# Kernel tuning notes

Measured on AMD Instinct MI355X. Metric: run time of the kernel, lower is better.

The kernel has to match this reference:

```python
import jax, jax.numpy as jnp
import numpy as np

ITERS = 8
LAMBDA0 = 0.01
PAD = 1.0
LR = 1.0
EPS = 1e-12


def _sobel_grads(fmap):
    # kornia spatial_gradient: normalized 3x3 sobel (/8), replicate padding. fmap: C,H,W
    kx = jnp.array([[-1., 0., 1.], [-2., 0., 2.], [-1., 0., 1.]], fmap.dtype) / 8.0
    k = jnp.stack([kx, kx.T])[:, None]                       # 2,1,3,3 (OIHW)
    f = jnp.pad(fmap, ((0, 0), (1, 1), (1, 1)), mode='edge')[:, None]  # C,1,H+2,W+2
    g = jax.lax.conv_general_dilated(f, k, (1, 1), 'VALID')  # C,2,H,W
    return g[:, 0], g[:, 1]


def _bilinear(tensor, pts):
    # grid_sample bilinear, align_corners=True, at pixel coords. tensor: C,H,W; pts: N,2 (x,y) -> N,C
    c, h, w = tensor.shape
    x, y = pts[:, 0], pts[:, 1]
    x0 = jnp.clip(jnp.floor(x), 0, w - 1)
    y0 = jnp.clip(jnp.floor(y), 0, h - 1)
    x1 = jnp.clip(x0 + 1, 0, w - 1)
    y1 = jnp.clip(y0 + 1, 0, h - 1)
    wx, wy = x - x0, y - y0
    x0i, x1i = x0.astype(jnp.int32), x1.astype(jnp.int32)
    y0i, y1i = y0.astype(jnp.int32), y1.astype(jnp.int32)
    v00 = tensor[:, y0i, x0i]
    v01 = tensor[:, y0i, x1i]
    v10 = tensor[:, y1i, x0i]
    v11 = tensor[:, y1i, x1i]
    out = (v00 * (1 - wx) * (1 - wy) + v01 * wx * (1 - wy)
           + v10 * (1 - wx) * wy + v11 * wx * wy)
    return out.T


def _skew(v):
    x, y, z = v[..., 0], v[..., 1], v[..., 2]
    o = jnp.zeros_like(x)
    return jnp.stack([o, -z, y, z, o, -x, -y, x, o], -1).reshape(v.shape[:-1] + (3, 3))


def _so3exp(w):
    theta = jnp.linalg.norm(w)
    small = theta < 1e-7
    th = jnp.where(small, 1.0, theta)
    A = jnp.where(small, 1.0, jnp.sin(th) / th)
    B = jnp.where(small, 0.5, (1.0 - jnp.cos(th)) / th ** 2)
    W = _skew(w)
    return jnp.eye(3, dtype=w.dtype) + A * W + B * (W @ W)


def _normalize(x):
    return x / jnp.maximum(jnp.linalg.norm(x, axis=-1, keepdims=True), EPS)


def _pnp(p3D, feature_ref, feature_query, K, R_init, t_init):
    C, H, W = feature_query.shape
    gx, gy = _sobel_grads(feature_query)
    fref = _normalize(feature_ref)
    fx, fy, cx, cy = K[0, 0], K[1, 1], K[0, 2], K[1, 2]
    f_scale = jnp.stack([fx, fy])
    c_off = jnp.stack([cx, cy])

    def project(R, t):
        p3q = p3D @ R.T + t
        pn = p3q[:, :2] / p3q[:, 2:3]
        return p3q, pn, pn * f_scale + c_off

    def in_image(p2):
        return ((p2[:, 0] >= PAD) & (p2[:, 0] < W - PAD)
                & (p2[:, 1] >= PAD) & (p2[:, 1] < H - PAD))

    def masked_cost(p2, vf):
        f = _normalize(_bilinear(feature_query, p2))
        cost = ((f - fref) ** 2).sum(-1)
        return (cost * vf).sum() / vf.sum()

    R, t = R_init, t_init
    lam = jnp.asarray(LAMBDA0, p3D.dtype)
    jacobi = None
    cost_best = None
    p2D_init = None

    for i in range(ITERS):
        p3q, pn, p2 = project(R, t)
        if i == 0:
            p2D_init = jax.lax.stop_gradient(p2)
        vf = in_image(p2).astype(p3D.dtype)  # mask-weight == gather of valid pts

        f_raw = _bilinear(feature_query, p2)  # N,C
        norm = jnp.maximum(jnp.linalg.norm(f_raw, axis=-1, keepdims=True), EPS)
        f = f_raw / norm
        error = f - fref
        if i == 0:
            cost_best = (((error ** 2).sum(-1)) * vf).sum() / vf.sum()

        # Jacobian chain: J = J_f_p2 @ J_p2_pn @ J_pn_p3 @ J_p3_T   -> N,C,6
        x_, y_, d = p3q[:, 0], p3q[:, 1], p3q[:, 2]
        z = jnp.zeros_like(d)
        Jpn = jnp.stack([1 / d, z, -x_ / d ** 2,
                         z, 1 / d, -y_ / d ** 2], -1).reshape(-1, 2, 3)
        Jpn = Jpn * f_scale[None, :, None]  # fold in J_p2_pn = diag(fx,fy)
        Jp3T = jnp.concatenate(
            [jnp.broadcast_to(jnp.eye(3, dtype=p3D.dtype), p3q.shape[:-1] + (3, 3)),
             -_skew(p3q)], -1)  # N,3,6
        J26 = Jpn @ Jp3T       # N,2,6

        Jf = jnp.stack([_bilinear(gx, p2), _bilinear(gy, p2)], -1)  # N,C,2
        # normalize-feat Jacobian (I - f f^T)/||f_raw||, fused (no NxCxC)
        proj = jnp.einsum('nc,nck->nk', f, Jf)
        Jf = (Jf - f[:, :, None] * proj[:, None, :]) / norm[:, :, None]

        J = Jf @ J26  # N,C,6
        if i == 0:
            jacobi = 1.0 / (1.0 + jnp.linalg.norm(J * vf[:, None, None], axis=(0, 1)))
        J = J * jacobi

        Grad = jnp.einsum('ncj,nc,n->j', J, error, vf)
        Hess = jnp.einsum('nci,ncj,n->ij', J, J, vf)

        damp = jnp.diag(jnp.diagonal(Hess) + 1e-9) * lam  # LM damping
        delta = -LR * jnp.linalg.solve(Hess + damp, Grad)
        delta = delta * jacobi
        dt, dw = delta[:3], delta[3:6]
        dr = _so3exp(dw)
        R_new, t_new = dr @ R, dr @ t + dt

        _, _, p2_new = project(R_new, t_new)
        vf_new = in_image(p2_new).astype(p3D.dtype)
        cost_new = masked_cost(p2_new, vf_new)

        accept = cost_new <= cost_best
        lam = jnp.clip(lam * jnp.where(accept, 0.1, 10.0), 1e-8, 1e4)
        R = jnp.where(accept, R_new, R)
        t = jnp.where(accept, t_new, t)
        cost_best = jnp.where(accept, cost_new, cost_best)

    p3D_sg = jax.lax.stop_gradient(p3D)
    pf = p3D_sg @ R.T + t
    p2f = (pf[:, :2] / pf[:, 2:3]) * f_scale + c_off
    f_i = _normalize(_bilinear(feature_query, p2D_init))
    f_f = _normalize(_bilinear(feature_query, p2f))
    cost_init = ((fref - f_i) ** 2).sum(-1)
    cost_final = ((fref - f_f) ** 2).sum(-1)
    nan = jnp.asarray(jnp.nan, cost_init.dtype)
    cost_init = jnp.where(in_image(p2D_init), cost_init, nan)
    cost_final = jnp.where(in_image(p2f), cost_final, nan)
    return R, t, cost_init, cost_final


def setup_inputs() -> dict:
    N, C, H, W = 10000, 128, 512, 512
    key = jax.random.key(0)
    ks = jax.random.split(key, 4)
    xy = jax.random.uniform(ks[0], (N, 2), jnp.float32, -2.0, 2.0)
    z = jax.random.uniform(ks[1], (N, 1), jnp.float32, 4.0, 10.0)
    p3D = jnp.concatenate([xy, z], -1)
    feature_query = jax.random.normal(ks[2], (C, H, W), jnp.float32) * 0.5
    feature_ref = jax.random.normal(ks[3], (N, C), jnp.float32)
    K = jnp.array([[500., 0., 256.], [0., 500., 256.], [0., 0., 1.]], jnp.float32)
    R_init = _so3exp(jnp.array([0.01, -0.02, 0.015], jnp.float32))
    t_init = jnp.array([0.05, -0.03, 0.10], jnp.float32)
    return {"p3D": p3D, "feature_ref": feature_ref, "feature_query": feature_query,
            "K": K, "R_init": R_init, "t_init": t_init}


def reference(p3D, feature_ref, feature_query, K, R_init, t_init):
    return _pnp(p3D, feature_ref, feature_query, K, R_init, t_init)
```

## Files before the change

### kernel.cpp

```cpp
#include <hip/hip_runtime.h>
#include <hip/hip_fp16.h>
#include <math.h>

#define HW_ (512*512)

typedef float vf4 __attribute__((ext_vector_type(4)));

__device__ __forceinline__ float wred(float v){
#pragma unroll
  for (int o = 32; o > 0; o >>= 1) v += __shfl_xor(v, o, 64);
  return v;
}

template<bool TR>
__device__ __forceinline__ float2 tap(const void* __restrict__ f, int y, int x, int c0){
  if (TR){
    const __half2* p = (const __half2*)f + (((size_t)((y << 9) + x)) << 6) + (c0 >> 1);
    return __half22float2(*p);
  } else {
    const float* ff = (const float*)f;
    int base = (y << 9) + x;
    float2 r;
    r.x = ff[(size_t)c0 * HW_ + base];
    r.y = ff[(size_t)(c0 + 1) * HW_ + base];
    return r;
  }
}

__device__ __forceinline__ void fgrad(const float P[16], float w00, float w01, float w10, float w11,
                                      float& f, float& gx, float& gy){
  f = w00*P[5] + w01*P[6] + w10*P[9] + w11*P[10];
  float gx11 = (P[2]  + 2.f*P[6]  + P[10] - P[0] - 2.f*P[4]  - P[8] ) * 0.125f;
  float gx12 = (P[3]  + 2.f*P[7]  + P[11] - P[1] - 2.f*P[5]  - P[9] ) * 0.125f;
  float gx21 = (P[6]  + 2.f*P[10] + P[14] - P[4] - 2.f*P[8]  - P[12]) * 0.125f;
  float gx22 = (P[7]  + 2.f*P[11] + P[15] - P[5] - 2.f*P[9]  - P[13]) * 0.125f;
  gx = w00*gx11 + w01*gx12 + w10*gx21 + w11*gx22;
  float gy11 = (P[8]  + 2.f*P[9]  + P[10] - P[0] - 2.f*P[1]  - P[2] ) * 0.125f;
  float gy12 = (P[9]  + 2.f*P[10] + P[11] - P[1] - 2.f*P[2]  - P[3] ) * 0.125f;
  float gy21 = (P[12] + 2.f*P[13] + P[14] - P[4] - 2.f*P[5]  - P[6] ) * 0.125f;
  float gy22 = (P[13] + 2.f*P[14] + P[15] - P[5] - 2.f*P[6]  - P[7] ) * 0.125f;
  gy = w00*gy11 + w01*gy12 + w10*gy21 + w11*gy22;
}

template<bool TR>
__device__ __forceinline__ float cost_point(const void* __restrict__ fmap,
                                            const float* __restrict__ frn,
                                            int n, float px, float py, int lane){
  int c0 = 2 * lane;
  float x0f = fminf(fmaxf(floorf(px), 0.f), 511.f);
  float y0f = fminf(fmaxf(floorf(py), 0.f), 511.f);
  int x0 = (int)x0f, y0 = (int)y0f;
  int x1 = min(x0 + 1, 511), y1 = min(y0 + 1, 511);
  float wx = px - x0f, wy = py - y0f;
  float w00 = (1.f-wx)*(1.f-wy), w01 = wx*(1.f-wy), w10 = (1.f-wx)*wy, w11 = wx*wy;
  float2 a = tap<TR>(fmap, y0, x0, c0), b = tap<TR>(fmap, y0, x1, c0);
  float2 c = tap<TR>(fmap, y1, x0, c0), d = tap<TR>(fmap, y1, x1, c0);
  float f0 = w00*a.x + w01*b.x + w10*c.x + w11*d.x;
  float f1 = w00*a.y + w01*b.y + w10*c.y + w11*d.y;
  const float2 fr = *(const float2*)(frn + (size_t)n*128 + c0);
  float Sff  = wred(f0*f0 + f1*f1);
  float Sffr = wred(f0*fr.x + f1*fr.y);
  float Sfr  = wred(fr.x*fr.x + fr.y*fr.y);
  float nrm = fmaxf(sqrtf(Sff), 1e-12f);
  float inv = 1.f / nrm;
  return Sff*inv*inv - 2.f*Sffr*inv + Sfr;
}

__global__ __launch_bounds__(256) void transpose_kernel(const float* __restrict__ fq,
                                                        __half* __restrict__ ftr){
  __shared__ float tf[256 * 32];
  int g  = blockIdx.x & 3;
  int sb = (blockIdx.x >> 2) << 8;
  int t = threadIdx.x;
  int l = t & 63, w = t >> 6;
  int s = l >> 4;
  int ipg = (l & 15) + (w << 4);
  int px0 = ipg << 2;
#pragma unroll
  for (int p = 0; p < 8; p++){
    int ch = s * 8 + p;
    const vf4* src = (const vf4*)(fq + (size_t)(g*32 + ch) * HW_ + sb + px0);
    vf4 v = __builtin_nontemporal_load(src);
#pragma unroll
    for (int j = 0; j < 4; j++){
      int px = px0 + j;
      int fz = ((3 * (px >> 2)) + ((px & 3) << 3)) & 31;
      tf[px * 32 + (ch ^ fz)] = v[j];
    }
  }
  __syncthreads();
#pragma unroll
  for (int q = 0; q < 4; q++){
    int px = (q << 6) + (t >> 2);
    int c8 = (t & 3) << 3;
    int fz = ((3 * (px >> 2)) + ((px & 3) << 3)) & 31;
    float v[8];
#pragma unroll
    for (int j = 0; j < 8; j++) v[j] = tf[px * 32 + ((c8 + j) ^ fz)];
    __half2 hh[4];
    hh[0] = __floats2half2_rn(v[0], v[1]);
    hh[1] = __floats2half2_rn(v[2], v[3]);
    hh[2] = __floats2half2_rn(v[4], v[5]);
    hh[3] = __floats2half2_rn(v[6], v[7]);
    *(uint4*)(ftr + ((size_t)(sb + px)) * 128 + g * 32 + c8) = *(uint4*)hh;
  }
}

__global__ __launch_bounds__(256) void prep_kernel(const float* __restrict__ fref,
                                                   float* __restrict__ frn,
                                                   const float* __restrict__ Rin,
                                                   const float* __restrict__ tin,
                                                   float* __restrict__ state, int N){
  if (blockIdx.x == 0){
    int t = threadIdx.x;
    if (t < 9) state[t] = Rin[t];
    if (t < 3) state[9 + t] = tin[t];
    if (t == 0) state[30] = 0.01f;
  }
  int lane = threadIdx.x & 63;
  int n = blockIdx.x * 4 + (threadIdx.x >> 6);
  if (n >= N) return;
  int c0 = 2 * lane;
  float2 fr = *(const float2*)(fref + (size_t)n*128 + c0);
  float rn = fmaxf(sqrtf(wred(fr.x*fr.x + fr.y*fr.y)), 1e-12f);
  float2 o; o.x = fr.x / rn; o.y = fr.y / rn;
  *(float2*)(frn + (size_t)n*128 + c0) = o;
}

template<bool TR>
__global__ __launch_bounds__(512) void eval_kernel(
    const float* __restrict__ p3D, const float* __restrict__ frn,
    const void* __restrict__ fmap, const float* __restrict__ Km,
    const float* __restrict__ state, int po, double* __restrict__ part,
    float* __restrict__ cost_out, int N)
{
  int t = threadIdx.x;
  int lane = t & 63;
  int wv = t >> 6;
  int n = blockIdx.x * 8 + wv;
  double acc = 0.0;
  if (n < N){
    float fx = Km[0], fy = Km[4], cx = Km[2], cy = Km[5];
    float R0=state[po+0],R1=state[po+1],R2=state[po+2],R3=state[po+3],R4=state[po+4];
    float R5=state[po+5],R6=state[po+6],R7=state[po+7],R8=state[po+8];
    float t0=state[po+9], t1=state[po+10], t2=state[po+11];
    float PX = p3D[3*n], PY = p3D[3*n+1], PZ = p3D[3*n+2];
    float X = R0*PX + R1*PY + R2*PZ + t0;
    float Y = R3*PX + R4*PY + R5*PZ + t1;
    float D = R6*PX + R7*PY + R8*PZ + t2;
    float px = X / D * fx + cx;
    float py = Y / D * fy + cy;
    bool valid = (px >= 1.f && px < 511.f && py >= 1.f && py < 511.f);
    if (valid){
      int c0 = 2 * lane;
      float x0f = fminf(fmaxf(floorf(px), 0.f), 511.f);
      float y0f = fminf(fmaxf(floorf(py), 0.f), 511.f);
      int x0 = (int)x0f, y0 = (int)y0f;
      int x1 = min(x0 + 1, 511), y1 = min(y0 + 1, 511);
      float wx = px - x0f, wy = py - y0f;
      int xs[4] = {max(x0-1,0), x0, x1, min(x1+1,511)};
      int ys[4] = {max(y0-1,0), y0, y1, min(y1+1,511)};
      float Pa[16], Pb[16];
#pragma unroll
      for (int r = 0; r < 4; r++)
#pragma unroll
        for (int scol = 0; scol < 4; scol++){
          float2 v = tap<TR>(fmap, ys[r], xs[scol], c0);
          Pa[r*4+scol] = v.x; Pb[r*4+scol] = v.y;
        }
      float w00 = (1.f-wx)*(1.f-wy), w01 = wx*(1.f-wy), w10 = (1.f-wx)*wy, w11 = wx*wy;
      float f0, gx0, gy0, f1, gx1, gy1;
      fgrad(Pa, w00, w01, w10, w11, f0, gx0, gy0);
      fgrad(Pb, w00, w01, w10, w11, f1, gx1, gy1);
      const float2 fr2 = *(const float2*)(frn + (size_t)n*128 + c0);
      float Sff   = wred(f0*f0   + f1*f1);
      float Sffr  = wred(f0*fr2.x + f1*fr2.y);
      float Sfr   = wred(fr2.x*fr2.x + fr2.y*fr2.y);
      float Sfgx  = wred(f0*gx0  + f1*gx1);
      float Sfgy  = wred(f0*gy0  + f1*gy1);
      float Sgxfr = wred(gx0*fr2.x + gx1*fr2.y);
      float Sgyfr = wred(gy0*fr2.x + gy1*fr2.y);
      float Sgxgx = wred(gx0*gx0 + gx1*gx1);
      float Sgxgy = wred(gx0*gy0 + gx1*gy1);
      float Sgygy = wred(gy0*gy0 + gy1*gy1);
      float nrm = fmaxf(sqrtf(Sff), 1e-12f);
      float inv = 1.f/nrm, inv2 = inv*inv, inv3 = inv2*inv, inv4 = inv2*inv2;
      float se2 = Sff*inv2 - 2.f*Sffr*inv + Sfr;
      float gex = Sfgx*inv2 - Sgxfr*inv - Sfgx*Sff*inv4 + Sfgx*Sffr*inv3;
      float gey = Sfgy*inv2 - Sgyfr*inv - Sfgy*Sff*inv4 + Sfgy*Sffr*inv3;
      float sxx = Sgxgx*inv2 - Sfgx*Sfgx*inv4;
      float sxy = Sgxgy*inv2 - Sfgx*Sfgy*inv4;
      float syy = Sgygy*inv2 - Sfgy*Sfgy*inv4;
      float invD = 1.f / D;
      float rx = X * invD, ry = Y * invD;
      float A[6] = {fx*invD, 0.f, -fx*rx*invD, -fx*rx*ry, fx*(1.f+rx*rx), -fx*ry};
      float B[6] = {0.f, fy*invD, -fy*ry*invD, -fy*(1.f+ry*ry), fy*rx*ry, fy*rx};
      int li = 0, lj = 0;
      {
        const int pi_[21] = {0,0,0,0,0,0,1,1,1,1,1,2,2,2,2,3,3,3,4,4,5};
        const int pj_[21] = {0,1,2,3,4,5,1,2,3,4,5,2,3,4,5,3,4,5,4,5,5};
        if (lane >= 6 && lane < 27){ li = pi_[lane-6]; lj = pj_[lane-6]; }
      }
      float val = 0.f;
      if (lane < 6)        val = A[lane]*gex + B[lane]*gey;
      else if (lane < 27)  val = A[li]*A[lj]*sxx + (A[li]*B[lj] + A[lj]*B[li])*sxy + B[li]*B[lj]*syy;
      else if (lane == 27) val = se2;
      else if (lane == 28) val = 1.f;
      acc = (double)val;
      if (cost_out && lane == 0) cost_out[n] = se2;
    } else if (cost_out && lane == 0){
      cost_out[n] = __int_as_float(0x7fc00000);
    }
  }
  __shared__ double red[8][32];
  if (lane < 32) red[wv][lane] = acc;
  __syncthreads();
  if (t < 32){
    double s = 0.0;
#pragma unroll
    for (int i = 0; i < 8; i++) s += red[i][t];
    part[(size_t)blockIdx.x * 32 + t] = s;
  }
}

template<bool TR>
__global__ __launch_bounds__(512) void cost7_kernel(
    const float* __restrict__ p3D, const float* __restrict__ frn,
    const void* __restrict__ fmap, const float* __restrict__ Km,
    const float* __restrict__ state, int po, double* __restrict__ part, int N)
{
  int t = threadIdx.x;
  int lane = t & 63;
  int wv = t >> 6;
  int n = blockIdx.x * 8 + wv;
  double acc = 0.0;
  if (n < N){
    float fx = Km[0], fy = Km[4], cx = Km[2], cy = Km[5];
    float PX = p3D[3*n], PY = p3D[3*n+1], PZ = p3D[3*n+2];
    float X = state[po+0]*PX + state[po+1]*PY + state[po+2]*PZ + state[po+9];
    float Y = state[po+3]*PX + state[po+4]*PY + state[po+5]*PZ + state[po+10];
    float D = state[po+6]*PX + state[po+7]*PY + state[po+8]*PZ + state[po+11];
    float px = X / D * fx + cx, py = Y / D * fy + cy;
    if (px >= 1.f && px < 511.f && py >= 1.f && py < 511.f){
      float cp = cost_point<TR>(fmap, frn, n, px, py, lane);
      if (lane == 27) acc = (double)cp;
      else if (lane == 28) acc = 1.0;
    }
  }
  __shared__ double red[8][32];
  if (lane < 32) red[wv][lane] = acc;
  __syncthreads();
  if (t < 32){
    double s = 0.0;
#pragma unroll
    for (int i = 0; i < 8; i++) s += red[i][t];
    part[(size_t)blockIdx.x * 32 + t] = s;
  }
}

__device__ void solve_step(const double* __restrict__ cur, float* __restrict__ state){
  const int pi_[21] = {0,0,0,0,0,0,1,1,1,1,1,2,2,2,2,3,3,3,4,4,5};
  const int pj_[21] = {0,1,2,3,4,5,1,2,3,4,5,2,3,4,5,3,4,5,4,5,5};
  double rg[6]; for (int i = 0; i < 6; i++) rg[i] = cur[i];
  double rh[6][6];
  for (int k = 0; k < 21; k++){ rh[pi_[k]][pj_[k]] = cur[6+k]; rh[pj_[k]][pi_[k]] = cur[6+k]; }
  float jac[6];
  for (int j = 0; j < 6; j++) jac[j] = state[24+j];
  double lam = (double)state[30];
  double H[6][7];
  for (int i = 0; i < 6; i++)
    for (int j = 0; j < 6; j++) H[i][j] = (double)jac[i] * (double)jac[j] * rh[i][j];
  for (int i = 0; i < 6; i++) H[i][i] += (H[i][i] + 1e-9) * lam;
  for (int i = 0; i < 6; i++) H[i][6] = -((double)jac[i] * rg[i]);
  for (int k = 0; k < 6; k++){
    int p = k; double mx = fabs(H[k][k]);
    for (int r = k+1; r < 6; r++) if (fabs(H[r][k]) > mx){ mx = fabs(H[r][k]); p = r; }
    if (p != k) for (int c = k; c < 7; c++){ double tmp = H[k][c]; H[k][c] = H[p][c]; H[p][c] = tmp; }
    double inv = 1.0 / H[k][k];
    for (int r = k+1; r < 6; r++){
      double m = H[r][k] * inv;
      for (int c = k; c < 7; c++) H[r][c] -= m * H[k][c];
    }
  }
  double d[6];
  for (int i = 5; i >= 0; i--){
    double sx = H[i][6];
    for (int c = i+1; c < 6; c++) sx -= H[i][c] * d[c];
    d[i] = sx / H[i][i];
  }
  for (int j = 0; j < 6; j++) d[j] *= (double)jac[j];
  double wx = d[3], wy = d[4], wz = d[5];
  double th2 = wx*wx + wy*wy + wz*wz, th = sqrt(th2);
  double Aa, Bb;
  if (th < 1e-7){ Aa = 1.0; Bb = 0.5; } else { Aa = sin(th)/th; Bb = (1.0 - cos(th))/th2; }
  double W[3][3] = {{0,-wz,wy},{wz,0,-wx},{-wy,wx,0}};
  double W2[3][3];
  for (int i = 0; i < 3; i++) for (int j = 0; j < 3; j++){
    double q = 0; for (int k = 0; k < 3; k++) q += W[i][k]*W[k][j]; W2[i][j] = q;
  }
  double dr[3][3];
  for (int i = 0; i < 3; i++) for (int j = 0; j < 3; j++)
    dr[i][j] = (i == j ? 1.0 : 0.0) + Aa*W[i][j] + Bb*W2[i][j];
  double Rc[3][3], tc[3];
  for (int i = 0; i < 3; i++){ tc[i] = state[9+i]; for (int j = 0; j < 3; j++) Rc[i][j] = state[i*3+j]; }
  for (int i = 0; i < 3; i++){
    for (int j = 0; j < 3; j++){
      double q = 0; for (int k = 0; k < 3; k++) q += dr[i][k]*Rc[k][j];
      state[12 + i*3 + j] = (float)q;
    }
    double q = 0; for (int k = 0; k < 3; k++) q += dr[i][k]*tc[k];
    state[21 + i] = (float)(q + d[i]);
  }
}

__global__ __launch_bounds__(1024) void update_kernel(
    const double* __restrict__ part, int rows, float* __restrict__ state,
    double* __restrict__ cur, int iter)
{
  __shared__ double sm[32*32];
  __shared__ double tot[32];
  int t = threadIdx.x;
  int l = t & 31, ch = t >> 5;
  double s = 0.0;
  for (int r = ch; r < rows; r += 32) s += part[(size_t)r*32 + l];
  sm[ch*32 + l] = s;
  __syncthreads();
  if (t < 32){
    double x = 0.0;
    for (int c = 0; c < 32; c++) x += sm[c*32 + t];
    tot[t] = x;
  }
  __syncthreads();
  if (t != 0) return;

  if (iter < 0){
    const int diag_k[6] = {0, 6, 11, 15, 18, 20};
    for (int j = 0; j < 6; j++)
      state[24+j] = 1.0f / (1.0f + (float)sqrt(tot[6 + diag_k[j]]));
    state[31] = (float)(tot[27] / tot[28]);
    for (int k = 0; k < 32; k++) cur[k] = tot[k];
    solve_step(cur, state);
  } else {
    float cn = (float)(tot[27] / tot[28]);
    bool acpt = (cn <= state[31]);
    float lam = state[30] * (acpt ? 0.1f : 10.f);
    state[30] = fminf(fmaxf(lam, 1e-8f), 1e4f);
    if (acpt){
      for (int i = 0; i < 12; i++) state[i] = state[12+i];
      state[31] = cn;
      for (int k = 0; k < 32; k++) cur[k] = tot[k];
    }
    if (iter < 7) solve_step(cur, state);
  }
}

template<bool TR>
__global__ __launch_bounds__(256) void final_kernel(
    const float* __restrict__ p3D, const float* __restrict__ frn,
    const void* __restrict__ fmap, const float* __restrict__ Km,
    const float* __restrict__ state, float* __restrict__ out, int N)
{
  if (blockIdx.x == 0 && threadIdx.x < 12) out[threadIdx.x] = state[threadIdx.x];
  int lane = threadIdx.x & 63;
  int n = blockIdx.x * 4 + (threadIdx.x >> 6);
  if (n >= N) return;
  float fx = Km[0], fy = Km[4], cx = Km[2], cy = Km[5];
  float PX = p3D[3*n], PY = p3D[3*n+1], PZ = p3D[3*n+2];
  float X = state[0]*PX + state[1]*PY + state[2]*PZ + state[9];
  float Y = state[3]*PX + state[4]*PY + state[5]*PZ + state[10];
  float D = state[6]*PX + state[7]*PY + state[8]*PZ + state[11];
  float px = X / D * fx + cx, py = Y / D * fy + cy;
  bool vf = (px >= 1.f && px < 511.f && py >= 1.f && py < 511.f);
  float cf = __int_as_float(0x7fc00000);
  if (vf) cf = cost_point<TR>(fmap, frn, n, px, py, lane);
  if (lane == 0) out[12 + N + n] = cf;
}

extern "C" void kernel_launch(void* const* d_in, const int* in_sizes, int n_in,
                              void* d_out, int out_size, void* d_ws, size_t ws_size,
                              hipStream_t stream)
{
  const float* p3D  = (const float*)d_in[0];
  const float* fref = (const float*)d_in[1];
  const float* fq   = (const float*)d_in[2];
  const float* Km   = (const float*)d_in[3];
  const float* Rin  = (const float*)d_in[4];
  const float* tin  = (const float*)d_in[5];
  float* out = (float*)d_out;
  int N = in_sizes[0] / 3;
  int NBLK  = (N + 7) / 8;
  int NBLK4 = (N + 3) / 4;

  char* w = (char*)d_ws;
  float*  state = (float*)w;
  double* cur   = (double*)(w + 256);
  double* part  = (double*)(w + 512);
  size_t part_bytes = (size_t)NBLK * 32 * 8;
  float* frn = (float*)(w + 512 + part_bytes);
  size_t frn_bytes = (size_t)N * 128 * 4;
  size_t ftr_off = (512 + part_bytes + frn_bytes + 255) & ~(size_t)255;
  __half* ftr = (__half*)(w + ftr_off);
  size_t need = ftr_off + (size_t)HW_ * 128 * 2;
  bool tr = (ws_size >= need);

  if (tr) transpose_kernel<<<(HW_/256)*4, 256, 0, stream>>>(fq, ftr);
  const void* fmap = tr ? (const void*)ftr : (const void*)fq;
  prep_kernel<<<NBLK4, 256, 0, stream>>>(fref, frn, Rin, tin, state, N);

  if (tr) eval_kernel<true ><<<NBLK, 512, 0, stream>>>(p3D, frn, fmap, Km, state, 0, part, out + 12, N);
  else    eval_kernel<false><<<NBLK, 512, 0, stream>>>(p3D, frn, fmap, Km, state, 0, part, out + 12, N);
  update_kernel<<<1, 1024, 0, stream>>>(part, NBLK, state, cur, -1);

  for (int it = 0; it < 7; it++){
    if (tr) eval_kernel<true ><<<NBLK, 512, 0, stream>>>(p3D, frn, fmap, Km, state, 12, part, nullptr, N);
    else    eval_kernel<false><<<NBLK, 512, 0, stream>>>(p3D, frn, fmap, Km, state, 12, part, nullptr, N);
    update_kernel<<<1, 1024, 0, stream>>>(part, NBLK, state, cur, it);
  }
  if (tr) cost7_kernel<true ><<<NBLK, 512, 0, stream>>>(p3D, frn, fmap, Km, state, 12, part, N);
  else    cost7_kernel<false><<<NBLK, 512, 0, stream>>>(p3D, frn, fmap, Km, state, 12, part, N);
  update_kernel<<<1, 1024, 0, stream>>>(part, NBLK, state, cur, 7);

  if (tr) final_kernel<true ><<<NBLK4, 256, 0, stream>>>(p3D, frn, fmap, Km, state, out, N);
  else    final_kernel<false><<<NBLK4, 256, 0, stream>>>(p3D, frn, fmap, Km, state, out, N);
}
```

Before: 471.6 us.

## Cache per-point 4x4 feature patches across LM iterations keyed by integer pixel

Adds a per-point cache of the gathered 4x4 half-precision feature patch, keyed by the integer top-left pixel (x0,y0). When a later iteration projects the point into the same cell, the eval kernel reads 4 contiguous uint4 per lane instead of 16 scattered gathers from the transposed feature map. On a miss it gathers as before and writes the patch and key to the cache, which adds N*4KB of workspace traffic. The values stay identical because the cached patch is the same fp16 data.

```diff
diff --git a/kernel.cpp b/kernel.cpp
--- a/kernel.cpp
+++ b/kernel.cpp
@@ -110,7 +110,8 @@
                                                    float* __restrict__ frn,
                                                    const float* __restrict__ Rin,
                                                    const float* __restrict__ tin,
-                                                   float* __restrict__ state, int N){
+                                                   float* __restrict__ state,
+                                                   int2* __restrict__ ckey, int N){
   if (blockIdx.x == 0){
     int t = threadIdx.x;
     if (t < 9) state[t] = Rin[t];
@@ -120,6 +121,7 @@
   int lane = threadIdx.x & 63;
   int n = blockIdx.x * 4 + (threadIdx.x >> 6);
   if (n >= N) return;
+  if (ckey && lane == 0){ int2 k; k.x = -1; k.y = -1; ckey[n] = k; }
   int c0 = 2 * lane;
   float2 fr = *(const float2*)(fref + (size_t)n*128 + c0);
   float rn = fmaxf(sqrtf(wred(fr.x*fr.x + fr.y*fr.y)), 1e-12f);
@@ -132,7 +134,8 @@
     const float* __restrict__ p3D, const float* __restrict__ frn,
     const void* __restrict__ fmap, const float* __restrict__ Km,
     const float* __restrict__ state, int po, double* __restrict__ part,
-    float* __restrict__ cost_out, int N)
+    float* __restrict__ cost_out, uint4* __restrict__ cache,
+    int2* __restrict__ ckey, int N)
 {
   int t = threadIdx.x;
   int lane = t & 63;
@@ -158,16 +161,51 @@
       int x0 = (int)x0f, y0 = (int)y0f;
       int x1 = min(x0 + 1, 511), y1 = min(y0 + 1, 511);
       float wx = px - x0f, wy = py - y0f;
-      int xs[4] = {max(x0-1,0), x0, x1, min(x1+1,511)};
-      int ys[4] = {max(y0-1,0), y0, y1, min(y1+1,511)};
       float Pa[16], Pb[16];
-#pragma unroll
-      for (int r = 0; r < 4; r++)
-#pragma unroll
-        for (int scol = 0; scol < 4; scol++){
-          float2 v = tap<TR>(fmap, ys[r], xs[scol], c0);
-          Pa[r*4+scol] = v.x; Pb[r*4+scol] = v.y;
+      bool hit = false;
+      if (TR && cache){
+        int2 k0 = ckey[n];
+        if (k0.x == x0 && k0.y == y0){
+          hit = true;
+          uint4 v[4];
+#pragma unroll
+          for (int j = 0; j < 4; j++) v[j] = cache[(size_t)n*256 + j*64 + lane];
+#pragma unroll
+          for (int j = 0; j < 4; j++){
+            unsigned u[4] = {v[j].x, v[j].y, v[j].z, v[j].w};
+#pragma unroll
+            for (int q = 0; q < 4; q++){
+              float2 vv = __half22float2(*(const __half2*)&u[q]);
+              Pa[j*4+q] = vv.x; Pb[j*4+q] = vv.y;
+            }
+          }
         }
+      }
+      if (!hit){
+        int xs[4] = {max(x0-1,0), x0, x1, min(x1+1,511)};
+        int ys[4] = {max(y0-1,0), y0, y1, min(y1+1,511)};
+#pragma unroll
+        for (int r = 0; r < 4; r++)
+#pragma unroll
+          for (int scol = 0; scol < 4; scol++){
+            float2 v = tap<TR>(fmap, ys[r], xs[scol], c0);
+            Pa[r*4+scol] = v.x; Pb[r*4+scol] = v.y;
+          }
+        if (TR && cache){
+#pragma unroll
+          for (int j = 0; j < 4; j++){
+            unsigned u[4];
+#pragma unroll
+            for (int q = 0; q < 4; q++){
+              __half2 h = __floats2half2_rn(Pa[j*4+q], Pb[j*4+q]);
+              u[q] = *(unsigned*)&h;
+            }
+            uint4 v; v.x = u[0]; v.y = u[1]; v.z = u[2]; v.w = u[3];
+            cache[(size_t)n*256 + j*64 + lane] = v;
+          }
+          if (lane == 0){ int2 nk; nk.x = x0; nk.y = y0; ckey[n] = nk; }
+        }
+      }
       float w00 = (1.f-wx)*(1.f-wy), w01 = wx*(1.f-wy), w10 = (1.f-wx)*wy, w11 = wx*wy;
       float f0, gx0, gy0, f1, gx1, gy1;
       fgrad(Pa, w00, w01, w10, w11, f0, gx0, gy0);
@@ -400,20 +438,26 @@
   size_t frn_bytes = (size_t)N * 128 * 4;
   size_t ftr_off = (512 + part_bytes + frn_bytes + 255) & ~(size_t)255;
   __half* ftr = (__half*)(w + ftr_off);
-  size_t need = ftr_off + (size_t)HW_ * 128 * 2;
-  bool tr = (ws_size >= need);
+  size_t need_tr = ftr_off + (size_t)HW_ * 128 * 2;
+  bool tr = (ws_size >= need_tr);
+  size_t cache_off = (need_tr + 255) & ~(size_t)255;
+  size_t ckey_off  = cache_off + (size_t)N * 4096;
+  size_t need_cache = ckey_off + (size_t)N * 8;
+  bool use_cache = tr && (ws_size >= need_cache);
+  uint4* cache = use_cache ? (uint4*)(w + cache_off) : nullptr;
+  int2*  ckey  = use_cache ? (int2*)(w + ckey_off)  : nullptr;
 
   if (tr) transpose_kernel<<<(HW_/256)*4, 256, 0, stream>>>(fq, ftr);
   const void* fmap = tr ? (const void*)ftr : (const void*)fq;
-  prep_kernel<<<NBLK4, 256, 0, stream>>>(fref, frn, Rin, tin, state, N);
-
-  if (tr) eval_kernel<true ><<<NBLK, 512, 0, stream>>>(p3D, frn, fmap, Km, state, 0, part, out + 12, N);
-  else    eval_kernel<false><<<NBLK, 512, 0, stream>>>(p3D, frn, fmap, Km, state, 0, part, out + 12, N);
+  prep_kernel<<<NBLK4, 256, 0, stream>>>(fref, frn, Rin, tin, state, ckey, N);
+
+  if (tr) eval_kernel<true ><<<NBLK, 512, 0, stream>>>(p3D, frn, fmap, Km, state, 0, part, out + 12, cache, ckey, N);
+  else    eval_kernel<false><<<NBLK, 512, 0, stream>>>(p3D, frn, fmap, Km, state, 0, part, out + 12, cache, ckey, N);
   update_kernel<<<1, 1024, 0, stream>>>(part, NBLK, state, cur, -1);
 
   for (int it = 0; it < 7; it++){
-    if (tr) eval_kernel<true ><<<NBLK, 512, 0, stream>>>(p3D, frn, fmap, Km, state, 12, part, nullptr, N);
-    else    eval_kernel<false><<<NBLK, 512, 0, stream>>>(p3D, frn, fmap, Km, state, 12, part, nullptr, N);
+    if (tr) eval_kernel<true ><<<NBLK, 512, 0, stream>>>(p3D, frn, fmap, Km, state, 12, part, nullptr, cache, ckey, N);
+    else    eval_kernel<false><<<NBLK, 512, 0, stream>>>(p3D, frn, fmap, Km, state, 12, part, nullptr, cache, ckey, N);
     update_kernel<<<1, 1024, 0, stream>>>(part, NBLK, state, cur, it);
   }
   if (tr) cost7_kernel<true ><<<NBLK, 512, 0, stream>>>(p3D, frn, fmap, Km, state, 12, part, N);
```

New measurement: 482.3 us. +2.3%, slower.
